# Kernel optimization log

Hardware: AMD Instinct MI355X
Metric: run time of the kernel (lower is better)

Reference implementation:

```python
import jax, jax.numpy as jnp
import numpy as np

N_NODES = 100_000
N_EDGES = 1_600_000
N_GRAPHS = 64
EPS = 1e-7  # GENConv message epsilon
D_IN, D_H, D_OUT, OUT_DIM = 128, 192, 128, 10


def _w(k, fan_in, fan_out):
    return jax.random.normal(k, (fan_in, fan_out), jnp.float32) * (1.0 / np.sqrt(fan_in))


def setup_inputs() -> dict:
    key = jax.random.key(0)
    ks = jax.random.split(key, 8)
    return {
        "x": jax.random.normal(ks[0], (N_NODES, D_IN), jnp.float32),
        "W0": _w(ks[1], D_IN, D_H), "b0": jnp.zeros((D_H,), jnp.float32),
        "W1": _w(ks[2], D_H, D_H), "b1": jnp.zeros((D_H,), jnp.float32),
        "W2": _w(ks[3], D_H, D_H), "b2": jnp.zeros((D_H,), jnp.float32),
        "W3": _w(ks[4], D_H, D_OUT), "b3": jnp.zeros((D_OUT,), jnp.float32),
        "Wfc": _w(ks[5], D_OUT, OUT_DIM), "bfc": jnp.zeros((OUT_DIM,), jnp.float32),
        "edge_index": jax.random.randint(ks[6], (2, N_EDGES), 0, N_NODES, jnp.int32),
        "batch": jnp.sort(jax.random.randint(ks[7], (N_NODES,), 0, N_GRAPHS, jnp.int32)),
    }


def _genconv(x, W, b, src, dst):
    # GENConv (num_layers=1, aggr='add'): message = relu(x_j) + eps,
    # scatter-add to dst, residual add, single Linear MLP.
    msg = jax.nn.relu(x[src]) + EPS          # [E, d]
    agg = jax.ops.segment_sum(msg, dst, num_segments=N_NODES)  # [N, d]
    return (x + agg) @ W + b


def reference(x, W0, b0, W1, b1, W2, b2, W3, b3, Wfc, bfc, edge_index, batch):
    src, dst = edge_index[0], edge_index[1]  # source_to_target flow
    for W, b in ((W0, b0), (W1, b1), (W2, b2), (W3, b3)):
        x = _genconv(x, W, b, src, dst)
    # global mean pool over graphs
    sums = jax.ops.segment_sum(x, batch, num_segments=N_GRAPHS)
    counts = jax.ops.segment_sum(jnp.ones((x.shape[0],), x.dtype), batch,
                                 num_segments=N_GRAPHS)
    pooled = sums / jnp.maximum(counts, 1.0)[:, None]  # [G, D_OUT]
    logits = pooled @ Wfc + bfc                        # [G, OUT_DIM]
    return jax.nn.log_softmax(logits, axis=1)
```

## Files before the change

### kernel.cpp

```cpp
#include <hip/hip_runtime.h>
#include <hip/hip_bf16.h>
#include <stdint.h>

constexpr int NN = 100000;
constexpr int NE = 1600000;
constexpr int NG = 64;
constexpr int S  = 192;
constexpr int NB_SCAN = 98;
constexpr unsigned int ZOFF = (unsigned int)NN * 384u;

constexpr int PREP_INDEG_BLK = 1563;
constexpr int PREP_CONVX_BLK = 12500;
constexpr int PREP_CONVW_BLK = 384;
constexpr int PREP_GB_BLK    = 391;
constexpr int PREP_GRID = PREP_INDEG_BLK + PREP_CONVX_BLK + PREP_CONVW_BLK + PREP_GB_BLK;

constexpr int EG_BLOCKS = 391;
constexpr int HROW = 50048;

typedef __bf16 bf16x8 __attribute__((ext_vector_type(8)));
typedef float  f32x16 __attribute__((ext_vector_type(16)));
typedef float  f32x2  __attribute__((ext_vector_type(2)));

union U16x4 { uint4 u; bf16x8 b; };

__device__ __forceinline__ float bl(unsigned int u) { return __uint_as_float(u << 16); }
__device__ __forceinline__ float bh(unsigned int u) { return __uint_as_float(u & 0xffff0000u); }
__device__ __forceinline__ float b16f(unsigned short u) { return __uint_as_float(((unsigned int)u) << 16); }
__device__ __forceinline__ unsigned int fb(float f) {
    unsigned int u = __float_as_uint(f);
    return (u + 0x7fffu + ((u >> 16) & 1u)) >> 16;
}
__device__ __forceinline__ unsigned int prelu(unsigned int u) {
    unsigned int r;
    asm("v_pk_max_f16 %0, %1, %2" : "=v"(r) : "v"(u), "v"(0u));
    return r;
}
__device__ __forceinline__ unsigned int cnt2bf(unsigned int h) {
    float f0 = (float)(h & 0xffffu);
    float f1 = (float)(h >> 16);
    return (__float_as_uint(f0) >> 16) | (__float_as_uint(f1) & 0xffff0000u);
}

__global__ __launch_bounds__(256) void k_prep(const float* __restrict__ x,
                                              const int* __restrict__ ei,
                                              const int* __restrict__ bat,
                                              const float* __restrict__ W0, const float* __restrict__ W1,
                                              const float* __restrict__ W2,
                                              unsigned short* __restrict__ A_,
                                              int* __restrict__ indeg, int* __restrict__ slot,
                                              unsigned short* __restrict__ T0, unsigned short* __restrict__ T1,
                                              unsigned short* __restrict__ T2,
                                              int* __restrict__ nstart) {
    const int b = blockIdx.x;
    if (b < PREP_INDEG_BLK) {
        int e4 = (b * 256 + threadIdx.x) * 4;
        if (e4 < NE) {
            int4 d = *(const int4*)(ei + NE + e4);
            int4 sl;
            sl.x = atomicAdd(&indeg[d.x], 1);
            sl.y = atomicAdd(&indeg[d.y], 1);
            sl.z = atomicAdd(&indeg[d.z], 1);
            sl.w = atomicAdd(&indeg[d.w], 1);
            *(int4*)(slot + e4) = sl;
        }
    } else if (b < PREP_INDEG_BLK + PREP_CONVX_BLK) {
        int id = (b - PREP_INDEG_BLK) * 256 + threadIdx.x;
        if (id < 96) ((unsigned int*)(A_ + (size_t)NN * S))[id] = 0u;
        int row = id >> 5, c4 = id & 31;
        float4 v = ((const float4*)x)[id];
        uint2 a;
        a.x = fb(v.x) | (fb(v.y) << 16);
        a.y = fb(v.z) | (fb(v.w) << 16);
        *(uint2*)(A_ + row * S + c4 * 4) = a;
    } else if (b < PREP_INDEG_BLK + PREP_CONVX_BLK + PREP_CONVW_BLK) {
        int id = (b - PREP_INDEG_BLK - PREP_CONVX_BLK) * 256 + threadIdx.x;
        const float* W; unsigned short* T; int N, base;
        if      (id < 24576) { W = W0; T = T0; N = 192; base = 0;     }
        else if (id < 61440) { W = W1; T = T1; N = 192; base = 24576; }
        else                 { W = W2; T = T2; N = 192; base = 61440; }
        int lid = id - base;
        int ci = lid >> 3, j = lid & 7;
        int kc = ci / N, n = ci % N;
        T[lid] = (unsigned short)fb(W[(kc * 8 + j) * N + n]);
    } else {
        int n = (b - PREP_INDEG_BLK - PREP_CONVX_BLK - PREP_CONVW_BLK) * 256 + threadIdx.x;
        if (n < NN) {
            int b0 = bat[n];
            int bprev = (n == 0) ? -1 : bat[n - 1];
            for (int g = bprev + 1; g <= b0; g++) nstart[g] = n;
            if (n == NN - 1)
                for (int g = b0 + 1; g < NG; g++) nstart[g] = NN;
        }
    }
}

__global__ __launch_bounds__(1024) void k_scan1(const int* __restrict__ indeg, int* __restrict__ offs,
                                                int* __restrict__ partials) {
    __shared__ int s[1024];
    int t = threadIdx.x;
    int gid = blockIdx.x * 1024 + t;
    int v = (gid < NN) ? indeg[gid] : 0;
    s[t] = v;
    __syncthreads();
    for (int d = 1; d < 1024; d <<= 1) {
        int tv = (t >= d) ? s[t - d] : 0;
        __syncthreads();
        s[t] += tv;
        __syncthreads();
    }
    if (gid < NN) offs[gid + 1] = s[t];
    if (t == 1023) partials[blockIdx.x] = s[1023];
}

__global__ __launch_bounds__(128) void k_scan2(int* __restrict__ offs, int* __restrict__ partials) {
    __shared__ int s[128];
    int t = threadIdx.x;
    int v = (t < NB_SCAN) ? partials[t] : 0;
    s[t] = v;
    __syncthreads();
    for (int d = 1; d < 128; d <<= 1) {
        int tv = (t >= d) ? s[t - d] : 0;
        __syncthreads();
        s[t] += tv;
        __syncthreads();
    }
    if (t < NB_SCAN) partials[t] = s[t] - v;
    if (t == 0) offs[0] = 0;
}

__device__ __forceinline__ int toff(const int* __restrict__ offs, const int* __restrict__ part, int j) {
    return j ? (offs[j] + part[(j - 1) >> 10]) : 0;
}

__global__ __launch_bounds__(256) void k_fill(const int* __restrict__ ei, const int* __restrict__ offs,
                                              const int* __restrict__ part,
                                              const int* __restrict__ slot, int* __restrict__ csr) {
    int e4 = (blockIdx.x * 256 + threadIdx.x) * 4;
    if (e4 >= NE) return;
    int4 sv = *(const int4*)(ei + e4);
    int4 dv = *(const int4*)(ei + NE + e4);
    int4 sl = *(const int4*)(slot + e4);
    csr[toff(offs, part, dv.x) + sl.x] = sv.x;
    csr[toff(offs, part, dv.y) + sl.y] = sv.y;
    csr[toff(offs, part, dv.z) + sl.z] = sv.z;
    csr[toff(offs, part, dv.w) + sl.w] = sv.w;
}

__global__ __launch_bounds__(256, 8) void k_agg192(const unsigned short* __restrict__ Ain,
                                                   unsigned short* __restrict__ Yout,
                                                   const int* __restrict__ offs,
                                                   const int* __restrict__ part,
                                                   const int* __restrict__ indeg,
                                                   const int* __restrict__ csr) {
    const int w = threadIdx.x >> 6, lane = threadIdx.x & 63;
    const int i = __builtin_amdgcn_readfirstlane(blockIdx.x * 4 + w);
    const bool act = lane < 48;
    const int deg   = __builtin_amdgcn_readfirstlane(indeg[i]);
    const int start = __builtin_amdgcn_readfirstlane(toff(offs, part, i));
    const int fo = (act ? lane : 47) * 8;
    const char* Ab = (const char*)Ain;

    f32x2 A01, A23;
    {
        uint2 p = *(const uint2*)(Ab + (size_t)i * 384 + fo);
        const float ed = 1e-7f * (float)deg;
        A01 = (f32x2){bl(p.x) + ed, bh(p.x) + ed};
        A23 = (f32x2){bl(p.y) + ed, bh(p.y) + ed};
    }

    const int* ecsr = csr + start;
    for (int e = 0; e < deg; e += 16) {
        unsigned int off[16];
#pragma unroll
        for (int k = 0; k < 16; k++) {
            int v = ecsr[e + k];
            off[k] = (e + k < deg) ? (unsigned int)v * 384u : ZOFF;
        }
        uint2 p[16];
#pragma unroll
        for (int k = 0; k < 16; k++)
            p[k] = *(const uint2*)(Ab + (size_t)off[k] + fo);
#pragma unroll
        for (int k = 0; k < 16; k++) {
            unsigned int rx = prelu(p[k].x), ry = prelu(p[k].y);
            A01 += (f32x2){bl(rx), bh(rx)};
            A23 += (f32x2){bl(ry), bh(ry)};
        }
    }
    if (act) {
        uint2 o;
        o.x = fb(A01.x) | (fb(A01.y) << 16);
        o.y = fb(A23.x) | (fb(A23.y) << 16);
        *(uint2*)(Yout + (size_t)i * S + lane * 4) = o;
    }
}

__global__ __launch_bounds__(256, 8) void k_agg128(const unsigned short* __restrict__ Ain,
                                                   unsigned short* __restrict__ Yout,
                                                   const int* __restrict__ offs,
                                                   const int* __restrict__ part,
                                                   const int* __restrict__ indeg,
                                                   const int* __restrict__ csr) {
    const int w = threadIdx.x >> 6, lane = threadIdx.x & 63;
    const int i = __builtin_amdgcn_readfirstlane(blockIdx.x * 4 + w);
    const int deg   = __builtin_amdgcn_readfirstlane(indeg[i]);
    const int start = __builtin_amdgcn_readfirstlane(toff(offs, part, i));
    const int fo = lane * 4;
    const char* Ab = (const char*)Ain;

    f32x2 A01;
    {
        unsigned int p = *(const unsigned int*)(Ab + (size_t)i * 384 + fo);
        const float ed = 1e-7f * (float)deg;
        A01 = (f32x2){bl(p) + ed, bh(p) + ed};
    }

    const int* ecsr = csr + start;
    for (int e = 0; e < deg; e += 16) {
        unsigned int off[16];
#pragma unroll
        for (int k = 0; k < 16; k++) {
            int v = ecsr[e + k];
            off[k] = (e + k < deg) ? (unsigned int)v * 384u : ZOFF;
        }
        unsigned int q[16];
#pragma unroll
        for (int k = 0; k < 16; k++)
            q[k] = *(const unsigned int*)(Ab + (size_t)off[k] + fo);
#pragma unroll
        for (int k = 0; k < 16; k++) {
            unsigned int r = prelu(q[k]);
            A01 += (f32x2){bl(r), bh(r)};
        }
    }
    *(unsigned int*)(Yout + (size_t)i * S + lane * 2) =
        fb(A01.x) | (fb(A01.y) << 16);
}

template <int K, int N>
__global__ __launch_bounds__(256) void k_gemm(const unsigned short* __restrict__ Yin,
                                              const unsigned short* __restrict__ WtC,
                                              const float* __restrict__ bias,
                                              unsigned short* __restrict__ Aout) {
    static_assert(K % 16 == 0 && N % 32 == 0, "");
    const int w = threadIdx.x >> 6, lane = threadIdx.x & 63;
    const int rt = blockIdx.x * 4 + w;
    if (rt >= (NN / 32)) return;
    const int hl = lane >> 5, lr = lane & 31;
    const int row0 = rt * 32;
    f32x16 acc[N / 32];
#pragma unroll
    for (int c = 0; c < N / 32; c++)
#pragma unroll
        for (int r = 0; r < 16; r++) acc[c][r] = 0.f;

    const unsigned short* ap = Yin + (row0 + lr) * S + hl * 8;
    const uint4* b4 = (const uint4*)WtC;
#pragma unroll
    for (int ks = 0; ks < K / 16; ks++) {
        U16x4 a;
        a.u = *(const uint4*)(ap + ks * 16);
#pragma unroll
        for (int c = 0; c < N / 32; c++) {
            U16x4 b;
            b.u = b4[(ks * 2 + hl) * N + c * 32 + lr];
            acc[c] = __builtin_amdgcn_mfma_f32_32x32x16_bf16(a.b, b.b, acc[c], 0, 0, 0);
        }
    }
#pragma unroll
    for (int c = 0; c < N / 32; c++) {
        const int col = c * 32 + lr;
        const float bc = bias[col];
#pragma unroll
        for (int r = 0; r < 16; r++) {
            const int row = row0 + (r & 3) + 8 * (r >> 2) + 4 * hl;
            Aout[row * S + col] = (unsigned short)fb(acc[c][r] + bc);
        }
    }
}

__global__ __launch_bounds__(256) void k_histpool(const int* __restrict__ csr,
                                                  const int* __restrict__ offs,
                                                  const int* __restrict__ part,
                                                  const int* __restrict__ nstart,
                                                  unsigned int* __restrict__ hist,
                                                  const unsigned short* __restrict__ X3,
                                                  const int* __restrict__ bat,
                                                  const int* __restrict__ indeg,
                                                  float* __restrict__ sums, float* __restrict__ cnt,
                                                  float* __restrict__ degsum) {
    const int b = blockIdx.x;
    if (b < 256) {
        const int g = b >> 2, q = b & 3;
        const int s0 = toff(offs, part, nstart[g]);
        const int s1 = (g == NG - 1) ? NE : toff(offs, part, nstart[g + 1]);
        const int len = s1 - s0;
        const int qs = s0 + (int)(((long long)len * q) >> 2);
        const int qe = s0 + (int)(((long long)len * (q + 1)) >> 2);
        unsigned int* hrow = hist + (size_t)g * HROW;
        for (int p = qs + threadIdx.x; p < qe; p += 256) {
            int src = csr[p];
            atomicAdd(&hrow[(unsigned int)src >> 1], 1u << (16 * (src & 1)));
        }
    } else {
        const int pb = b - 256;
        const int f = threadIdx.x;
        if (f >= 192) return;
        int n0 = pb * 50;
        int n1 = min(n0 + 50, NN);
        int cur = bat[n0];
        float acc = 0.f;
        int run = 0, dacc = 0;
        for (int n = n0; n < n1; n++) {
            int g = bat[n];
            if (g != cur) {
                atomicAdd(&sums[cur * 192 + f], acc);
                if (f == 0) { atomicAdd(&cnt[cur], (float)run); atomicAdd(&degsum[cur], (float)dacc); }
                acc = 0.f; run = 0; dacc = 0; cur = g;
            }
            acc += b16f(X3[(size_t)n * S + f]);
            run++;
            if (f == 0) dacc += indeg[n];
        }
        atomicAdd(&sums[cur * 192 + f], acc);
        if (f == 0) { atomicAdd(&cnt[cur], (float)run); atomicAdd(&degsum[cur], (float)dacc); }
    }
}

__global__ __launch_bounds__(384) void k_egemm(const unsigned short* __restrict__ X3,
                                               const unsigned int* __restrict__ hist,
                                               float* __restrict__ partials) {
    const int wv = threadIdx.x >> 6, lane = threadIdx.x & 63;
    const int b = blockIdx.x;
    const int j0 = b * 256;
    const int hl = lane >> 5, lr = lane & 31;
    const int feat = wv * 32 + lr;
    f32x16 acc[2];
#pragma unroll
    for (int m = 0; m < 2; m++)
#pragma unroll
        for (int r = 0; r < 16; r++) acc[m][r] = 0.f;

    for (int kk = 0; kk < 16; kk++) {
        const int jh = (j0 >> 1) + kk * 8 + hl * 4;
        U16x4 af[2];
#pragma unroll
        for (int m = 0; m < 2; m++) {
            uint4 h = *(const uint4*)(hist + (size_t)(m * 32 + lr) * HROW + jh);
            af[m].u = (uint4){cnt2bf(h.x), cnt2bf(h.y), cnt2bf(h.z), cnt2bf(h.w)};
        }
        U16x4 bf;
#pragma unroll
        for (int tp = 0; tp < 4; tp++) {
            int je = j0 + kk * 16 + hl * 8 + tp * 2;
            int ja = min(je, NN), jb = min(je + 1, NN);
            unsigned int u0 = X3[(size_t)ja * S + feat];
            unsigned int u1 = X3[(size_t)jb * S + feat];
            ((unsigned int*)&bf.u)[tp] = prelu(u0 | (u1 << 16));
        }
#pragma unroll
        for (int m = 0; m < 2; m++)
            acc[m] = __builtin_amdgcn_mfma_f32_32x32x16_bf16(af[m].b, bf.b, acc[m], 0, 0, 0);
    }
    float* pb = partials + (size_t)b * 12288;
#pragma unroll
    for (int m = 0; m < 2; m++)
#pragma unroll
        for (int r = 0; r < 16; r++) {
            const int g = m * 32 + (r & 3) + 8 * (r >> 2) + 4 * hl;
            pb[g * 192 + feat] = acc[m][r];
        }
}

__global__ __launch_bounds__(192) void k_head(const float* __restrict__ sums,
                                              const float* __restrict__ partials,
                                              const float* __restrict__ cnt, const float* __restrict__ degsum,
                                              const float* __restrict__ W3, const float* __restrict__ b3,
                                              const float* __restrict__ Wfc, const float* __restrict__ bfc,
                                              float* __restrict__ out) {
    __shared__ float py[192];
    __shared__ float tl[128];
    __shared__ float lg[10];
    const int g = blockIdx.x, t = threadIdx.x;
    const float inv = 1.f / fmaxf(cnt[g], 1.f);
    const float ed = 1e-7f * degsum[g];
    const float* pp = partials + g * 192 + t;
    float s0 = 0.f, s1 = 0.f, s2 = 0.f, s3 = 0.f;
    int p = 0;
    for (; p + 4 <= EG_BLOCKS; p += 4) {
        s0 += pp[(size_t)(p + 0) * 12288];
        s1 += pp[(size_t)(p + 1) * 12288];
        s2 += pp[(size_t)(p + 2) * 12288];
        s3 += pp[(size_t)(p + 3) * 12288];
    }
    for (; p < EG_BLOCKS; p++) s0 += pp[(size_t)p * 12288];
    py[t] = (sums[g * 192 + t] + ((s0 + s1) + (s2 + s3)) + ed) * inv;
    __syncthreads();
    if (t < 128) {
        float tf = b3[t];
        for (int k = 0; k < 192; k++) tf += py[k] * W3[k * 128 + t];
        tl[t] = tf;
    }
    __syncthreads();
    if (t < 10) {
        float s = bfc[t];
        for (int f = 0; f < 128; f++) s += tl[f] * Wfc[f * 10 + t];
        lg[t] = s;
    }
    __syncthreads();
    if (t < 10) {
        float m = lg[0];
        for (int k = 1; k < 10; k++) m = fmaxf(m, lg[k]);
        float se = 0.f;
        for (int k = 0; k < 10; k++) se += expf(lg[k] - m);
        out[g * 10 + t] = lg[t] - m - logf(se);
    }
}

constexpr size_t A0_OFF     = 0;
constexpr size_t A1_OFF     = 38400384;
constexpr size_t HIST_REL   = 0;
constexpr size_t PARTS_REL  = 12812288;
constexpr size_t CSR_OFF    = 76800384;
constexpr size_t OFFS_OFF   = 83200384;
constexpr size_t INDEG_OFF  = 83600512;
constexpr size_t SUMS_OFF   = 84000512;
constexpr size_t CNT_OFF    = 84049664;
constexpr size_t DEGS_OFF   = 84049920;
constexpr size_t PART_OFF   = 84050176;
constexpr size_t NSTART_OFF = 84050688;
constexpr size_t WT0_OFF    = 84050944;
constexpr size_t WT1_OFF    = 84100096;
constexpr size_t WT2_OFF    = 84173824;

extern "C" void kernel_launch(void* const* d_in, const int* in_sizes, int n_in,
                              void* d_out, int out_size, void* d_ws, size_t ws_size,
                              hipStream_t stream) {
    const float* x   = (const float*)d_in[0];
    const float* W0  = (const float*)d_in[1];
    const float* b0  = (const float*)d_in[2];
    const float* W1  = (const float*)d_in[3];
    const float* b1  = (const float*)d_in[4];
    const float* W2  = (const float*)d_in[5];
    const float* b2  = (const float*)d_in[6];
    const float* W3  = (const float*)d_in[7];
    const float* b3  = (const float*)d_in[8];
    const float* Wfc = (const float*)d_in[9];
    const float* bfc = (const float*)d_in[10];
    const int*   ei  = (const int*)d_in[11];
    const int*   bat = (const int*)d_in[12];
    float* out = (float*)d_out;

    char* ws = (char*)d_ws;
    unsigned short* A0  = (unsigned short*)(ws + A0_OFF);
    unsigned short* A1  = (unsigned short*)(ws + A1_OFF);
    int* slot   = (int*)(ws + A1_OFF);
    unsigned int* hist  = (unsigned int*)(ws + A1_OFF + HIST_REL);
    float* parts        = (float*)(ws + A1_OFF + PARTS_REL);
    int* csr    = (int*)(ws + CSR_OFF);
    int* offs   = (int*)(ws + OFFS_OFF);
    int* indeg  = (int*)(ws + INDEG_OFF);
    int* part   = (int*)(ws + PART_OFF);
    int* nstart = (int*)(ws + NSTART_OFF);
    unsigned short* Wt0 = (unsigned short*)(ws + WT0_OFF);
    unsigned short* Wt1 = (unsigned short*)(ws + WT1_OFF);
    unsigned short* Wt2 = (unsigned short*)(ws + WT2_OFF);
    float* sums   = (float*)(ws + SUMS_OFF);
    float* cnt    = (float*)(ws + CNT_OFF);
    float* degsum = (float*)(ws + DEGS_OFF);

    hipMemsetAsync(ws + INDEG_OFF, 0, 449664, stream);

    k_prep<<<PREP_GRID, 256, 0, stream>>>(x, ei, bat, W0, W1, W2, A0, indeg, slot,
                                          Wt0, Wt1, Wt2, nstart);

    k_scan1<<<NB_SCAN, 1024, 0, stream>>>(indeg, offs, part);
    k_scan2<<<1, 128, 0, stream>>>(offs, part);
    k_fill<<<(NE / 4 + 255) / 256, 256, 0, stream>>>(ei, offs, part, slot, csr);

    const int AGG_GRID  = NN / 4;
    const int GEMM_GRID = (NN / 32 + 3) / 4;

    k_agg128<<<AGG_GRID, 256, 0, stream>>>(A0, A1, offs, part, indeg, csr);
    k_gemm<128, 192><<<GEMM_GRID, 256, 0, stream>>>(A1, Wt0, b0, A0);
    k_agg192<<<AGG_GRID, 256, 0, stream>>>(A0, A1, offs, part, indeg, csr);
    k_gemm<192, 192><<<GEMM_GRID, 256, 0, stream>>>(A1, Wt1, b1, A0);
    k_agg192<<<AGG_GRID, 256, 0, stream>>>(A0, A1, offs, part, indeg, csr);
    k_gemm<192, 192><<<GEMM_GRID, 256, 0, stream>>>(A1, Wt2, b2, A0);

    hipMemsetAsync(ws + A1_OFF + HIST_REL, 0, 12812288, stream);
    k_histpool<<<2256, 256, 0, stream>>>(csr, offs, part, nstart, hist, A0, bat, indeg,
                                         sums, cnt, degsum);
    k_egemm<<<EG_BLOCKS, 384, 0, stream>>>(A0, hist, parts);
    k_head<<<NG, 192, 0, stream>>>(sums, parts, cnt, degsum, W3, b3, Wfc, bfc, out);
}
```

Measured before the change: 646.7 us.

## Fold partial-scan into fill kernel and zero histogram inside histpool

Drops the k_scan2 launch: every k_fill block now redoes the 98-entry scan of block partials in shared memory, and block 0 writes the exclusive result to a new part2 buffer that later kernels read. It also drops the 12.8 MB histogram memset: each histpool block zeroes its own quarter of a graph's histogram row. Each block now walks all of that graph's edges and only counts sources whose bin falls in its quarter. This cuts two launches and a large memset, at the cost of a redundant scan in every fill block and four times more CSR reads in the histogram stage. offs[0] is no longer set to 0 by the removed kernel, but toff short-circuits j=0, so this appears harmless.

```diff
diff --git a/kernel.cpp b/kernel.cpp
--- a/kernel.cpp
+++ b/kernel.cpp
@@ -17,6 +17,7 @@
 
 constexpr int EG_BLOCKS = 391;
 constexpr int HROW = 50048;
+constexpr int QROW = HROW / 4;
 
 typedef __bf16 bf16x8 __attribute__((ext_vector_type(8)));
 typedef float  f32x16 __attribute__((ext_vector_type(16)));
@@ -113,38 +114,42 @@
     if (t == 1023) partials[blockIdx.x] = s[1023];
 }
 
-__global__ __launch_bounds__(128) void k_scan2(int* __restrict__ offs, int* __restrict__ partials) {
+__device__ __forceinline__ int toff(const int* __restrict__ offs, const int* __restrict__ part, int j) {
+    return j ? (offs[j] + part[(j - 1) >> 10]) : 0;
+}
+
+__global__ __launch_bounds__(256) void k_fill(const int* __restrict__ ei, const int* __restrict__ offs,
+                                              const int* __restrict__ praw,
+                                              const int* __restrict__ slot, int* __restrict__ csr,
+                                              int* __restrict__ part2) {
     __shared__ int s[128];
-    int t = threadIdx.x;
-    int v = (t < NB_SCAN) ? partials[t] : 0;
-    s[t] = v;
+    __shared__ int spx[128];
+    const int t = threadIdx.x;
+    int v = 0;
+    if (t < 128) {
+        v = (t < NB_SCAN) ? praw[t] : 0;
+        s[t] = v;
+    }
     __syncthreads();
     for (int d = 1; d < 128; d <<= 1) {
-        int tv = (t >= d) ? s[t - d] : 0;
+        int tv = (t < 128 && t >= d) ? s[t - d] : 0;
         __syncthreads();
-        s[t] += tv;
+        if (t < 128) s[t] += tv;
         __syncthreads();
     }
-    if (t < NB_SCAN) partials[t] = s[t] - v;
-    if (t == 0) offs[0] = 0;
-}
-
-__device__ __forceinline__ int toff(const int* __restrict__ offs, const int* __restrict__ part, int j) {
-    return j ? (offs[j] + part[(j - 1) >> 10]) : 0;
-}
-
-__global__ __launch_bounds__(256) void k_fill(const int* __restrict__ ei, const int* __restrict__ offs,
-                                              const int* __restrict__ part,
-                                              const int* __restrict__ slot, int* __restrict__ csr) {
-    int e4 = (blockIdx.x * 256 + threadIdx.x) * 4;
+    if (t < 128) spx[t] = s[t] - v;
+    __syncthreads();
+    if (blockIdx.x == 0 && t < NB_SCAN) part2[t] = spx[t];
+
+    int e4 = (blockIdx.x * 256 + t) * 4;
     if (e4 >= NE) return;
     int4 sv = *(const int4*)(ei + e4);
     int4 dv = *(const int4*)(ei + NE + e4);
     int4 sl = *(const int4*)(slot + e4);
-    csr[toff(offs, part, dv.x) + sl.x] = sv.x;
-    csr[toff(offs, part, dv.y) + sl.y] = sv.y;
-    csr[toff(offs, part, dv.z) + sl.z] = sv.z;
-    csr[toff(offs, part, dv.w) + sl.w] = sv.w;
+    csr[(dv.x ? offs[dv.x] + spx[(dv.x - 1) >> 10] : 0) + sl.x] = sv.x;
+    csr[(dv.y ? offs[dv.y] + spx[(dv.y - 1) >> 10] : 0) + sl.y] = sv.y;
+    csr[(dv.z ? offs[dv.z] + spx[(dv.z - 1) >> 10] : 0) + sl.z] = sv.z;
+    csr[(dv.w ? offs[dv.w] + spx[(dv.w - 1) >> 10] : 0) + sl.w] = sv.w;
 }
 
 __global__ __launch_bounds__(256, 8) void k_agg192(const unsigned short* __restrict__ Ain,
@@ -293,15 +298,17 @@
     const int b = blockIdx.x;
     if (b < 256) {
         const int g = b >> 2, q = b & 3;
+        unsigned int* hrow = hist + (size_t)g * HROW;
+        const unsigned int q0 = q * QROW;
+        for (int i = threadIdx.x; i < QROW; i += 256) hrow[q0 + i] = 0u;
+        __syncthreads();
         const int s0 = toff(offs, part, nstart[g]);
         const int s1 = (g == NG - 1) ? NE : toff(offs, part, nstart[g + 1]);
-        const int len = s1 - s0;
-        const int qs = s0 + (int)(((long long)len * q) >> 2);
-        const int qe = s0 + (int)(((long long)len * (q + 1)) >> 2);
-        unsigned int* hrow = hist + (size_t)g * HROW;
-        for (int p = qs + threadIdx.x; p < qe; p += 256) {
+        for (int p = s0 + threadIdx.x; p < s1; p += 256) {
             int src = csr[p];
-            atomicAdd(&hrow[(unsigned int)src >> 1], 1u << (16 * (src & 1)));
+            unsigned int h = (unsigned int)src >> 1;
+            if (h - q0 < (unsigned int)QROW)
+                atomicAdd(&hrow[h], 1u << (16 * (src & 1)));
         }
     } else {
         const int pb = b - 256;
@@ -404,9 +411,9 @@
     }
     __syncthreads();
     if (t < 10) {
-        float s = bfc[t];
-        for (int f = 0; f < 128; f++) s += tl[f] * Wfc[f * 10 + t];
-        lg[t] = s;
+        float sf = bfc[t];
+        for (int f = 0; f < 128; f++) sf += tl[f] * Wfc[f * 10 + t];
+        lg[t] = sf;
     }
     __syncthreads();
     if (t < 10) {
@@ -429,10 +436,11 @@
 constexpr size_t CNT_OFF    = 84049664;
 constexpr size_t DEGS_OFF   = 84049920;
 constexpr size_t PART_OFF   = 84050176;
-constexpr size_t NSTART_OFF = 84050688;
-constexpr size_t WT0_OFF    = 84050944;
-constexpr size_t WT1_OFF    = 84100096;
-constexpr size_t WT2_OFF    = 84173824;
+constexpr size_t PART2_OFF  = 84050688;
+constexpr size_t NSTART_OFF = 84051200;
+constexpr size_t WT0_OFF    = 84051456;
+constexpr size_t WT1_OFF    = 84100608;
+constexpr size_t WT2_OFF    = 84174336;
 
 extern "C" void kernel_launch(void* const* d_in, const int* in_sizes, int n_in,
                               void* d_out, int out_size, void* d_ws, size_t ws_size,
@@ -462,6 +470,7 @@
     int* offs   = (int*)(ws + OFFS_OFF);
     int* indeg  = (int*)(ws + INDEG_OFF);
     int* part   = (int*)(ws + PART_OFF);
+    int* part2  = (int*)(ws + PART2_OFF);
     int* nstart = (int*)(ws + NSTART_OFF);
     unsigned short* Wt0 = (unsigned short*)(ws + WT0_OFF);
     unsigned short* Wt1 = (unsigned short*)(ws + WT1_OFF);
@@ -476,21 +485,19 @@
                                           Wt0, Wt1, Wt2, nstart);
 
     k_scan1<<<NB_SCAN, 1024, 0, stream>>>(indeg, offs, part);
-    k_scan2<<<1, 128, 0, stream>>>(offs, part);
-    k_fill<<<(NE / 4 + 255) / 256, 256, 0, stream>>>(ei, offs, part, slot, csr);
+    k_fill<<<(NE / 4 + 255) / 256, 256, 0, stream>>>(ei, offs, part, slot, csr, part2);
 
     const int AGG_GRID  = NN / 4;
     const int GEMM_GRID = (NN / 32 + 3) / 4;
 
-    k_agg128<<<AGG_GRID, 256, 0, stream>>>(A0, A1, offs, part, indeg, csr);
+    k_agg128<<<AGG_GRID, 256, 0, stream>>>(A0, A1, offs, part2, indeg, csr);
     k_gemm<128, 192><<<GEMM_GRID, 256, 0, stream>>>(A1, Wt0, b0, A0);
-    k_agg192<<<AGG_GRID, 256, 0, stream>>>(A0, A1, offs, part, indeg, csr);
+    k_agg192<<<AGG_GRID, 256, 0, stream>>>(A0, A1, offs, part2, indeg, csr);
     k_gemm<192, 192><<<GEMM_GRID, 256, 0, stream>>>(A1, Wt1, b1, A0);
-    k_agg192<<<AGG_GRID, 256, 0, stream>>>(A0, A1, offs, part, indeg, csr);
+    k_agg192<<<AGG_GRID, 256, 0, stream>>>(A0, A1, offs, part2, indeg, csr);
     k_gemm<192, 192><<<GEMM_GRID, 256, 0, stream>>>(A1, Wt2, b2, A0);
 
-    hipMemsetAsync(ws + A1_OFF + HIST_REL, 0, 12812288, stream);
-    k_histpool<<<2256, 256, 0, stream>>>(csr, offs, part, nstart, hist, A0, bat, indeg,
+    k_histpool<<<2256, 256, 0, stream>>>(csr, offs, part2, nstart, hist, A0, bat, indeg,
                                          sums, cnt, degsum);
     k_egemm<<<EG_BLOCKS, 384, 0, stream>>>(A0, hist, parts);
     k_head<<<NG, 192, 0, stream>>>(sums, parts, cnt, degsum, W3, b3, Wfc, bfc, out);
```

After: 647.9 us. No clear change (+0.2%).
